# Kernel tuning notes

Measured on AMD Instinct MI355X. Metric: run time of the kernel, lower is better.

## Reference

```python
import jax, jax.numpy as jnp
from jax import lax
import numpy as np

C = 768      # embed_dim
H = 8        # num_heads
SR = 2       # sr_ratio
EPS = 1e-5


def setup_inputs() -> dict:
    key = jax.random.key(0)
    ks = jax.random.split(key, 8)
    B, n = 1, 24
    N = n ** 3  # 13824
    s = 0.02
    x = jax.random.normal(ks[0], (B, N, C), jnp.float32)
    wq = jax.random.normal(ks[1], (C, C), jnp.float32) * s          # query (no bias)
    wkv = jax.random.normal(ks[2], (C, 2 * C), jnp.float32) * s     # key_value (no bias)
    sr_w = jax.random.normal(ks[3], (C, C, SR, SR, SR), jnp.float32) * s  # Conv3d OIDHW
    sr_b = jax.random.normal(ks[4], (C,), jnp.float32) * s
    ln_g = jnp.ones((C,), jnp.float32)
    ln_b = jnp.zeros((C,), jnp.float32)
    proj_w = jax.random.normal(ks[5], (C, C), jnp.float32) * s
    proj_b = jax.random.normal(ks[6], (C,), jnp.float32) * s
    return {"x": x, "wq": wq, "wkv": wkv, "sr_w": sr_w, "sr_b": sr_b,
            "ln_g": ln_g, "ln_b": ln_b, "proj_w": proj_w, "proj_b": proj_b}


def reference(x, wq, wkv, sr_w, sr_b, ln_g, ln_b, proj_w, proj_b):
    B, N, Cdim = x.shape
    d = Cdim // H
    n = round(N ** (1.0 / 3.0))
    # q: [B,H,N,d]
    q = (x @ wq).reshape(B, N, H, d).transpose(0, 2, 1, 3)
    # spatial reduction: conv3d with kernel=stride=SR
    x_ = x.transpose(0, 2, 1).reshape(B, Cdim, n, n, n)
    x_ = lax.conv_general_dilated(x_, sr_w, (SR, SR, SR), 'VALID',
                                  dimension_numbers=('NCDHW', 'OIDHW', 'NCDHW'))
    x_ = x_ + sr_b[None, :, None, None, None]
    x_ = x_.reshape(B, Cdim, -1).transpose(0, 2, 1)  # [B, N', C]
    mu = x_.mean(-1, keepdims=True)
    var = x_.var(-1, keepdims=True)
    x_ = (x_ - mu) / jnp.sqrt(var + EPS) * ln_g + ln_b
    # kv: [2,B,H,N',d]
    kv = (x_ @ wkv).reshape(B, -1, 2, H, d).transpose(2, 0, 3, 1, 4)
    k, v = kv[0], kv[1]
    # NOTE: original scales by sqrt(num_heads), not sqrt(head_dim) -- kept faithfully.
    scores = jnp.einsum('bhqd,bhkd->bhqk', q, k) / jnp.sqrt(jnp.float32(H))
    probs = jax.nn.softmax(scores, axis=-1)
    out = jnp.einsum('bhqk,bhkd->bhqd', probs, v)
    out = out.transpose(0, 2, 1, 3).reshape(B, N, Cdim)
    return out @ proj_w + proj_b
```

## Files before the change

### kernel.cpp

```cpp
#include <hip/hip_runtime.h>
#include <hip/hip_bf16.h>

typedef __hip_bfloat16 bf16;
typedef unsigned short u16;

#define CD 768
#define HH 8
#define HD 96
#define NT 13824
#define NR 1728
#define KCONV 6144

typedef __attribute__((ext_vector_type(8))) __bf16 bf16x8;
typedef __attribute__((ext_vector_type(8))) unsigned short us8;
typedef __attribute__((ext_vector_type(4))) unsigned short us4;
typedef __attribute__((ext_vector_type(4))) float floatx4;

#define OFF_XB   0L
#define OFF_Q    21233664L
#define OFF_XR   42467328L
#define OFF_XLN  47775744L
#define OFF_WQT  50429952L
#define OFF_WKVT 51609600L
#define OFF_PRJT 53968896L
#define OFF_SRWR 55148544L
#define OFF_PRB  64587264L
#define OFF_FLAG 64588800L

__device__ __forceinline__ float b2f(bf16 v) { return __bfloat162float(v); }
__device__ __forceinline__ floatx4 mfma16(bf16x8 a, bf16x8 b, floatx4 c) {
    return __builtin_amdgcn_mfma_f32_16x16x32_bf16(a, b, c, 0, 0, 0);
}
__device__ __forceinline__ u16 f2bf_bits(float x) {
    return __builtin_bit_cast(u16, __float2bfloat16(x));
}
__device__ __forceinline__ float ldin(const void* p, long i, int bf) {
    return bf ? b2f(((const bf16*)p)[i]) : ((const float*)p)[i];
}

__global__ void detect_kernel(const unsigned short* __restrict__ g, int* __restrict__ flag) {
    *flag = (g[0] == 0x3F80) ? 1 : 0;
}

__global__ __launch_bounds__(256) void cvt_kernel(
    const void* __restrict__ src, bf16* __restrict__ dst, long nchunk,
    const int* __restrict__ flagp)
{
    const int bf = *flagp;
    long c = (long)blockIdx.x * 256 + threadIdx.x;
    if (c >= nchunk) return;
    if (bf) {
        ((us8*)dst)[c] = ((const us8*)src)[c];
    } else {
        const float* s = (const float*)src + c * 8;
        us8 o;
#pragma unroll
        for (int j = 0; j < 8; ++j) o[j] = f2bf_bits(s[j]);
        ((us8*)dst)[c] = o;
    }
}

__global__ __launch_bounds__(256) void trans_kernel(
    const void* __restrict__ src, bf16* __restrict__ dst, int R, int Cc,
    const int* __restrict__ flagp)
{
    const int bf = *flagp;
    __shared__ float tile[32][33];
    const int tx = threadIdx.x & 31, ty = threadIdx.x >> 5;
    const int bx = blockIdx.x * 32, by = blockIdx.y * 32;
#pragma unroll
    for (int rr = 0; rr < 4; ++rr)
        tile[ty + rr * 8][tx] = ldin(src, (long)(by + ty + rr * 8) * Cc + bx + tx, bf);
    __syncthreads();
#pragma unroll
    for (int rr = 0; rr < 4; ++rr)
        dst[(long)(bx + ty + rr * 8) * R + by + tx] =
            __float2bfloat16(tile[tx][ty + rr * 8]);
}

__global__ __launch_bounds__(256) void reorder_srw_kernel(
    const void* __restrict__ src, bf16* __restrict__ dst,
    const int* __restrict__ flagp)
{
    const int bf = *flagp;
    const long total = 768L * 6144;
    for (long e = (long)blockIdx.x * 256 + threadIdx.x; e < total;
         e += (long)gridDim.x * 256) {
        long o = e / 6144;
        int rem = (int)(e - o * 6144);
        int tap = rem / 768, i = rem - tap * 768;
        dst[e] = __float2bfloat16(ldin(src, o * 6144 + i * 8 + tap, bf));
    }
}

template <bool GATHER, bool BIAS, int DST, int SPLITK, bool PRESCALE>
__global__ __launch_bounds__(256) void gemm_mfma(
    const bf16* __restrict__ A, const bf16* __restrict__ Bt,
    const bf16* __restrict__ bias, void* __restrict__ C, bf16* __restrict__ C2,
    int M, int N, int K, const int* __restrict__ flagp)
{
    const int bf = (DST == 0) ? *flagp : 0;
    __shared__ u16 Al[128][40];
    __shared__ u16 Bl[128][40];
    const int tid  = threadIdx.x;
    const int wave = tid >> 6, lane = tid & 63;
    const int l15  = lane & 15, quad = lane >> 4;
    const int m0 = blockIdx.y * 128, n0 = blockIdx.x * 128;
    const int mw = (wave & 1) * 64, nw = (wave >> 1) * 64;
    const int srow = tid >> 1, koff = (tid & 1) * 16;

    const int mclamp = min(m0 + srow, M - 1);
    int tokbase = 0;
    if (GATHER) {
        int zo = mclamp / 144, yo = (mclamp / 12) % 12, xo = mclamp % 12;
        tokbase = zo * 1152 + yo * 48 + xo * 2;
    }
    const long arow_off = (long)mclamp * K;
    const long brow_off = (long)(n0 + srow) * K;

    floatx4 acc[4][4];
#pragma unroll
    for (int mi = 0; mi < 4; ++mi)
#pragma unroll
        for (int ni = 0; ni < 4; ++ni) acc[mi][ni] = (floatx4){0.f, 0.f, 0.f, 0.f};

    const int ksteps = K >> 5;
    const int kchunk = ksteps / SPLITK;
    const int kb0 = (SPLITK > 1) ? blockIdx.z * kchunk : 0;
    for (int kb = kb0; kb < kb0 + kchunk; ++kb) {
        const bf16* asrc;
        if (GATHER) {
            int kk0 = kb << 5;
            int tap = kk0 / 768;
            int i0  = kk0 - tap * 768 + koff;
            int tok = tokbase + (tap >> 2) * 576 + ((tap >> 1) & 1) * 24 + (tap & 1);
            asrc = A + (long)tok * 768 + i0;
        } else {
            asrc = A + arow_off + (kb << 5) + koff;
        }
        us8 a0 = *(const us8*)asrc;
        us8 a1 = *(const us8*)(asrc + 8);
        us8 b0 = *(const us8*)(Bt + brow_off + (kb << 5) + koff);
        us8 b1 = *(const us8*)(Bt + brow_off + (kb << 5) + koff + 8);
        __syncthreads();
        *(us8*)&Al[srow][koff]     = a0;
        *(us8*)&Al[srow][koff + 8] = a1;
        *(us8*)&Bl[srow][koff]     = b0;
        *(us8*)&Bl[srow][koff + 8] = b1;
        __syncthreads();

        bf16x8 af[4], bfr[4];
#pragma unroll
        for (int mi = 0; mi < 4; ++mi)
            af[mi] = *(const bf16x8*)&Al[mw + mi * 16 + l15][quad * 8];
#pragma unroll
        for (int ni = 0; ni < 4; ++ni)
            bfr[ni] = *(const bf16x8*)&Bl[nw + ni * 16 + l15][quad * 8];
#pragma unroll
        for (int mi = 0; mi < 4; ++mi)
#pragma unroll
            for (int ni = 0; ni < 4; ++ni)
                acc[mi][ni] = mfma16(af[mi], bfr[ni], acc[mi][ni]);
    }

#pragma unroll
    for (int mi = 0; mi < 4; ++mi) {
        int rowb = m0 + mw + mi * 16 + quad * 4;
#pragma unroll
        for (int ni = 0; ni < 4; ++ni) {
            int col = n0 + nw + ni * 16 + l15;
            float bv = BIAS ? b2f(bias[col]) : 0.f;
#pragma unroll
            for (int r = 0; r < 4; ++r) {
                int row = rowb + r;
                if (row < M) {
                    float v = acc[mi][ni][r] + bv;
                    if (PRESCALE) v *= 0.35355339059327373f;
                    long idx = (long)row * N + col;
                    if (DST == 2)      ((float*)C)[idx] = v;
                    else if (DST == 1) ((bf16*)C)[idx] = __float2bfloat16(v);
                    else if (DST == 3) {
                        if (col < 768) ((bf16*)C)[(long)row * 768 + col] = __float2bfloat16(v);
                        else           C2[(long)(col - 768) * NR + row] = __float2bfloat16(v);
                    } else if (DST == 4) {
                        atomicAdd((float*)C + idx, v);
                    } else {
                        if (bf) ((bf16*)C)[idx] = __float2bfloat16(v);
                        else    ((float*)C)[idx] = v;
                    }
                }
            }
        }
    }
}

__global__ __launch_bounds__(256) void ln_kernel(
    const float* __restrict__ Xr, const void* __restrict__ srb,
    const void* __restrict__ g, const void* __restrict__ b,
    bf16* __restrict__ Xln, const int* __restrict__ flagp)
{
    const int bf = *flagp;
    __shared__ float red[256];
    __shared__ float mu_s, rs_s;
    const int t = blockIdx.x, tid = threadIdx.x;
    const float* row = Xr + (long)t * CD;
    float v0 = row[tid]       + ldin(srb, tid, bf);
    float v1 = row[tid + 256] + ldin(srb, tid + 256, bf);
    float v2 = row[tid + 512] + ldin(srb, tid + 512, bf);
    red[tid] = v0 + v1 + v2;
    __syncthreads();
    for (int off = 128; off; off >>= 1) {
        if (tid < off) red[tid] += red[tid + off];
        __syncthreads();
    }
    if (tid == 0) mu_s = red[0] * (1.0f / CD);
    __syncthreads();
    float mu = mu_s;
    float d0 = v0 - mu, d1 = v1 - mu, d2 = v2 - mu;
    red[tid] = d0 * d0 + d1 * d1 + d2 * d2;
    __syncthreads();
    for (int off = 128; off; off >>= 1) {
        if (tid < off) red[tid] += red[tid + off];
        __syncthreads();
    }
    if (tid == 0) rs_s = rsqrtf(red[0] * (1.0f / CD) + 1e-5f);
    __syncthreads();
    float rs = rs_s;
    bf16* orow = Xln + (long)t * CD;
    orow[tid]       = __float2bfloat16(d0 * rs * ldin(g, tid, bf)       + ldin(b, tid, bf));
    orow[tid + 256] = __float2bfloat16(d1 * rs * ldin(g, tid + 256, bf) + ldin(b, tid + 256, bf));
    orow[tid + 512] = __float2bfloat16(d2 * rs * ldin(g, tid + 512, bf) + ldin(b, tid + 512, bf));
}

__global__ __launch_bounds__(256) void attn_mfma_kernel(
    const bf16* __restrict__ Qg, const bf16* __restrict__ Kg,
    const bf16* __restrict__ VTg, bf16* __restrict__ Og)
{
    __shared__ u16 Ks[64][104];
    __shared__ u16 Vt[96][72];
    __shared__ u16 PT[4][32][72];

    const int tid  = threadIdx.x;
    const int wave = tid >> 6;
    const int lane = tid & 63;
    const int l15  = lane & 15;
    const int quad = lane >> 4;
    const int h    = blockIdx.y;
    const int q0   = blockIdx.x * 128 + wave * 32;

    bf16x8 bq[2][3];
#pragma unroll
    for (int qc = 0; qc < 2; ++qc)
#pragma unroll
        for (int kc = 0; kc < 3; ++kc)
            bq[qc][kc] = *(const bf16x8*)(Qg + (long)(q0 + qc * 16 + l15) * CD
                                          + h * HD + kc * 32 + quad * 8);

    floatx4 o[2][6];
    float lp[2] = {0.f, 0.f};
#pragma unroll
    for (int qc = 0; qc < 2; ++qc)
#pragma unroll
        for (int dc = 0; dc < 6; ++dc) o[qc][dc] = (floatx4){0.f, 0.f, 0.f, 0.f};

    const int stok = tid >> 2;
    const int dseg = (tid & 3) * 24;

    for (int kt = 0; kt < NR; kt += 64) {
        __syncthreads();
        {
            const u16* krow = (const u16*)Kg + (long)(kt + stok) * 768 + h * HD;
#pragma unroll
            for (int s = 0; s < 3; ++s)
                *(us8*)&Ks[stok][dseg + s * 8] = *(const us8*)(krow + dseg + s * 8);
#pragma unroll
            for (int i = 0; i < 3; ++i) {
                int unit = i * 256 + tid;
                int dim = unit >> 3, t8 = (unit & 7) << 3;
                *(us8*)&Vt[dim][t8] =
                    *(const us8*)((const u16*)VTg + (long)(h * HD + dim) * NR + kt + t8);
            }
        }
        __syncthreads();

#pragma unroll
        for (int tc = 0; tc < 4; ++tc) {
            bf16x8 ak[3];
#pragma unroll
            for (int kc = 0; kc < 3; ++kc)
                ak[kc] = *(const bf16x8*)&Ks[tc * 16 + l15][kc * 32 + quad * 8];
#pragma unroll
            for (int qc = 0; qc < 2; ++qc) {
                floatx4 acc = {0.f, 0.f, 0.f, 0.f};
#pragma unroll
                for (int kc = 0; kc < 3; ++kc) acc = mfma16(ak[kc], bq[qc][kc], acc);
                float e0 = __expf(acc[0]), e1 = __expf(acc[1]);
                float e2 = __expf(acc[2]), e3 = __expf(acc[3]);
                lp[qc] += (e0 + e1) + (e2 + e3);
                us4 p4;
                p4[0] = f2bf_bits(e0); p4[1] = f2bf_bits(e1);
                p4[2] = f2bf_bits(e2); p4[3] = f2bf_bits(e3);
                *(us4*)&PT[wave][qc * 16 + l15][tc * 16 + quad * 4] = p4;
            }
        }

#pragma unroll
        for (int ks = 0; ks < 2; ++ks) {
            bf16x8 ap[2];
#pragma unroll
            for (int qc = 0; qc < 2; ++qc)
                ap[qc] = *(const bf16x8*)&PT[wave][qc * 16 + l15][ks * 32 + quad * 8];
#pragma unroll
            for (int dc = 0; dc < 6; ++dc) {
                bf16x8 bv = *(const bf16x8*)&Vt[dc * 16 + l15][ks * 32 + quad * 8];
#pragma unroll
                for (int qc = 0; qc < 2; ++qc)
                    o[qc][dc] = mfma16(ap[qc], bv, o[qc][dc]);
            }
        }
    }

#pragma unroll
    for (int qc = 0; qc < 2; ++qc) {
        float ls = lp[qc];
        ls += __shfl_xor(ls, 16);
        ls += __shfl_xor(ls, 32);
        float inv = 1.0f / ls;
#pragma unroll
        for (int r = 0; r < 4; ++r) {
            float invr = __shfl(inv, quad * 4 + r, 16);
            int row = q0 + qc * 16 + quad * 4 + r;
#pragma unroll
            for (int dc = 0; dc < 6; ++dc)
                Og[(long)row * CD + h * HD + dc * 16 + l15] =
                    __float2bfloat16(o[qc][dc][r] * invr);
        }
    }
}

extern "C" void kernel_launch(void* const* d_in, const int* in_sizes, int n_in,
                              void* d_out, int out_size, void* d_ws, size_t ws_size,
                              hipStream_t stream) {
    const void* x      = d_in[0];
    const void* wq     = d_in[1];
    const void* wkv    = d_in[2];
    const void* sr_w   = d_in[3];
    const void* sr_b   = d_in[4];
    const void* ln_g   = d_in[5];
    const void* ln_b   = d_in[6];
    const void* proj_w = d_in[7];
    const void* proj_b = d_in[8];

    char* ws = (char*)d_ws;
    bf16*  xb    = (bf16*)(ws + OFF_XB);
    bf16*  O     = (bf16*)(ws + OFF_XB);
    bf16*  Q     = (bf16*)(ws + OFF_Q);
    float* Xr    = (float*)(ws + OFF_XR);
    bf16*  Kg    = (bf16*)(ws + OFF_XR);
    bf16*  VTg   = (bf16*)(ws + OFF_XR + 2654208);
    bf16*  Xln   = (bf16*)(ws + OFF_XLN);
    bf16*  wqT   = (bf16*)(ws + OFF_WQT);
    bf16*  wkvT  = (bf16*)(ws + OFF_WKVT);
    bf16*  prjT  = (bf16*)(ws + OFF_PRJT);
    bf16*  srwR  = (bf16*)(ws + OFF_SRWR);
    bf16*  prbB  = (bf16*)(ws + OFF_PRB);
    int*   flag  = (int*)(ws + OFF_FLAG);

    detect_kernel<<<1, 1, 0, stream>>>((const unsigned short*)ln_g, flag);
    cvt_kernel<<<5184, 256, 0, stream>>>(x, xb, (long)NT * CD / 8, flag);
    trans_kernel<<<dim3(24, 24), 256, 0, stream>>>(wq, wqT, CD, CD, flag);
    trans_kernel<<<dim3(48, 24), 256, 0, stream>>>(wkv, wkvT, CD, 1536, flag);
    trans_kernel<<<dim3(24, 24), 256, 0, stream>>>(proj_w, prjT, CD, CD, flag);
    reorder_srw_kernel<<<4608, 256, 0, stream>>>(sr_w, srwR, flag);
    cvt_kernel<<<1, 256, 0, stream>>>(proj_b, prbB, CD / 8, flag);

    hipMemsetAsync(Xr, 0, (long)NR * CD * 4, stream);
    gemm_mfma<true, false, 4, 4, false><<<dim3(6, 14, 4), 256, 0, stream>>>(
        xb, srwR, nullptr, Xr, nullptr, NR, CD, KCONV, flag);
    ln_kernel<<<NR, 256, 0, stream>>>(Xr, sr_b, ln_g, ln_b, Xln, flag);
    gemm_mfma<false, false, 3, 1, false><<<dim3(12, 14), 256, 0, stream>>>(
        Xln, wkvT, nullptr, Kg, VTg, NR, 1536, CD, flag);
    gemm_mfma<false, false, 1, 1, true><<<dim3(6, 108), 256, 0, stream>>>(
        xb, wqT, nullptr, Q, nullptr, NT, CD, CD, flag);
    attn_mfma_kernel<<<dim3(NT / 128, HH), 256, 0, stream>>>(Q, Kg, VTg, O);
    gemm_mfma<false, true, 0, 1, false><<<dim3(6, 108), 256, 0, stream>>>(
        O, prjT, prbB, d_out, nullptr, NT, CD, CD, flag);
}
```

Measured before the change: 434.4 us.

## Prefetch next K/V tile into registers and swizzle attention block order

The attention kernel now loads the next 64-token K and V^T tile into registers while computing on the current tile in shared memory, so global loads overlap with MFMA work instead of stalling between barriers. The block-to-(head, query block) mapping is also remapped so consecutively launched blocks interleave heads, likely to spread each head's K/V reads across XCDs/L2 differently. This adds register pressure from 6 extra 128-bit registers per thread, which could reduce occupancy.

```diff
diff --git a/kernel.cpp b/kernel.cpp
--- a/kernel.cpp
+++ b/kernel.cpp
@@ -245,8 +245,12 @@
     const int lane = tid & 63;
     const int l15  = lane & 15;
     const int quad = lane >> 4;
-    const int h    = blockIdx.y;
-    const int q0   = blockIdx.x * 128 + wave * 32;
+
+    const int lin  = blockIdx.y * 108 + blockIdx.x;
+    const int nid  = (lin & 7) * 108 + (lin >> 3);
+    const int h    = nid / 108;
+    const int qblk = nid - h * 108;
+    const int q0   = qblk * 128 + wave * 32;
 
     bf16x8 bq[2][3];
 #pragma unroll
@@ -265,23 +269,33 @@
 
     const int stok = tid >> 2;
     const int dseg = (tid & 3) * 24;
+    const int vdim = tid >> 3;
+    const int vt8  = (tid & 7) << 3;
+    const u16* kbase = (const u16*)Kg + (long)stok * 768 + h * HD + dseg;
+    const u16* vbase = (const u16*)VTg + (long)(h * HD + vdim) * NR + vt8;
+
+    us8 kreg[3], vreg[3];
+#pragma unroll
+    for (int s = 0; s < 3; ++s) kreg[s] = *(const us8*)(kbase + s * 8);
+#pragma unroll
+    for (int i = 0; i < 3; ++i) vreg[i] = *(const us8*)(vbase + (long)i * 32 * NR);
 
     for (int kt = 0; kt < NR; kt += 64) {
         __syncthreads();
-        {
-            const u16* krow = (const u16*)Kg + (long)(kt + stok) * 768 + h * HD;
-#pragma unroll
-            for (int s = 0; s < 3; ++s)
-                *(us8*)&Ks[stok][dseg + s * 8] = *(const us8*)(krow + dseg + s * 8);
-#pragma unroll
-            for (int i = 0; i < 3; ++i) {
-                int unit = i * 256 + tid;
-                int dim = unit >> 3, t8 = (unit & 7) << 3;
-                *(us8*)&Vt[dim][t8] =
-                    *(const us8*)((const u16*)VTg + (long)(h * HD + dim) * NR + kt + t8);
-            }
-        }
-        __syncthreads();
+#pragma unroll
+        for (int s = 0; s < 3; ++s) *(us8*)&Ks[stok][dseg + s * 8] = kreg[s];
+#pragma unroll
+        for (int i = 0; i < 3; ++i) *(us8*)&Vt[vdim + i * 32][vt8] = vreg[i];
+        __syncthreads();
+
+        if (kt + 64 < NR) {
+            const u16* k2 = kbase + (long)(kt + 64) * 768;
+            const u16* v2 = vbase + (kt + 64);
+#pragma unroll
+            for (int s = 0; s < 3; ++s) kreg[s] = *(const us8*)(k2 + s * 8);
+#pragma unroll
+            for (int i = 0; i < 3; ++i) vreg[i] = *(const us8*)(v2 + (long)i * 32 * NR);
+        }
 
 #pragma unroll
         for (int tc = 0; tc < 4; ++tc) {
```

After: 423.2 us. -2.6%, faster.

## Load K/V fragments straight from global memory and remap blocks so heads share XCDs

Applied to the files above, without the earlier changes.

Drops the shared-memory staging of K and V tiles and the two block barriers per key tile. Each wave now reads its MFMA operand fragments directly from global memory and relies on L2 for reuse across the four waves. The block index is also remapped so that blocks of the same head land together, likely on the same XCD, to improve L2 locality of K/V. The trade is that each wave now issues redundant global loads instead of sharing one LDS copy, with higher latency that the compiler has to hide.

```diff
diff --git a/kernel.cpp b/kernel.cpp
--- a/kernel.cpp
+++ b/kernel.cpp
@@ -236,8 +236,6 @@
     const bf16* __restrict__ Qg, const bf16* __restrict__ Kg,
     const bf16* __restrict__ VTg, bf16* __restrict__ Og)
 {
-    __shared__ u16 Ks[64][104];
-    __shared__ u16 Vt[96][72];
     __shared__ u16 PT[4][32][72];
 
     const int tid  = threadIdx.x;
@@ -245,8 +243,12 @@
     const int lane = tid & 63;
     const int l15  = lane & 15;
     const int quad = lane >> 4;
-    const int h    = blockIdx.y;
-    const int q0   = blockIdx.x * 128 + wave * 32;
+
+    const int lin  = blockIdx.y * 108 + blockIdx.x;
+    const int nid  = (lin & 7) * 108 + (lin >> 3);
+    const int h    = nid / 108;
+    const int qblk = nid - h * 108;
+    const int q0   = qblk * 128 + wave * 32;
 
     bf16x8 bq[2][3];
 #pragma unroll
@@ -263,32 +265,17 @@
 #pragma unroll
         for (int dc = 0; dc < 6; ++dc) o[qc][dc] = (floatx4){0.f, 0.f, 0.f, 0.f};
 
-    const int stok = tid >> 2;
-    const int dseg = (tid & 3) * 24;
+    const u16* kfrag = (const u16*)Kg + (long)l15 * CD + h * HD + quad * 8;
+    const u16* vfrag = (const u16*)VTg + (long)(h * HD + l15) * NR + quad * 8;
 
     for (int kt = 0; kt < NR; kt += 64) {
-        __syncthreads();
-        {
-            const u16* krow = (const u16*)Kg + (long)(kt + stok) * 768 + h * HD;
-#pragma unroll
-            for (int s = 0; s < 3; ++s)
-                *(us8*)&Ks[stok][dseg + s * 8] = *(const us8*)(krow + dseg + s * 8);
-#pragma unroll
-            for (int i = 0; i < 3; ++i) {
-                int unit = i * 256 + tid;
-                int dim = unit >> 3, t8 = (unit & 7) << 3;
-                *(us8*)&Vt[dim][t8] =
-                    *(const us8*)((const u16*)VTg + (long)(h * HD + dim) * NR + kt + t8);
-            }
-        }
-        __syncthreads();
-
 #pragma unroll
         for (int tc = 0; tc < 4; ++tc) {
             bf16x8 ak[3];
+            const u16* kp = kfrag + (long)(kt + tc * 16) * CD;
 #pragma unroll
             for (int kc = 0; kc < 3; ++kc)
-                ak[kc] = *(const bf16x8*)&Ks[tc * 16 + l15][kc * 32 + quad * 8];
+                ak[kc] = *(const bf16x8*)(kp + kc * 32);
 #pragma unroll
             for (int qc = 0; qc < 2; ++qc) {
                 floatx4 acc = {0.f, 0.f, 0.f, 0.f};
@@ -312,7 +299,7 @@
                 ap[qc] = *(const bf16x8*)&PT[wave][qc * 16 + l15][ks * 32 + quad * 8];
 #pragma unroll
             for (int dc = 0; dc < 6; ++dc) {
-                bf16x8 bv = *(const bf16x8*)&Vt[dc * 16 + l15][ks * 32 + quad * 8];
+                bf16x8 bv = *(const bf16x8*)(vfrag + (long)(dc * 16) * NR + kt + ks * 32);
 #pragma unroll
                 for (int qc = 0; qc < 2; ++qc)
                     o[qc][dc] = mfma16(ap[qc], bv, o[qc][dc]);
```

Result: slower. 606.6 us (+39.6%).
